# Performance work log

Measured on AMD Instinct MI355X. Metric: run time of the kernel, lower is better.

The kernel has to match this reference:

```python
import jax, jax.numpy as jnp
import numpy as np

H_DIM = 1024
HEAD_SIZE = 1024


def setup_inputs() -> dict:
    key = jax.random.key(0)
    ks = jax.random.split(key, 7)
    s = 1.0 / np.sqrt(H_DIM)
    x = jax.random.normal(ks[0], (4, 4096, H_DIM), dtype=jnp.float32)
    Wq = jax.random.uniform(ks[1], (H_DIM, HEAD_SIZE), jnp.float32, -s, s)
    bq = jax.random.uniform(ks[2], (HEAD_SIZE,), jnp.float32, -s, s)
    Wk = jax.random.uniform(ks[3], (H_DIM, HEAD_SIZE), jnp.float32, -s, s)
    bk = jax.random.uniform(ks[4], (HEAD_SIZE,), jnp.float32, -s, s)
    Wv = jax.random.uniform(ks[5], (H_DIM, HEAD_SIZE), jnp.float32, -s, s)
    bv = jax.random.uniform(ks[6], (HEAD_SIZE,), jnp.float32, -s, s)
    return {"x": x, "Wq": Wq, "bq": bq, "Wk": Wk, "bk": bk, "Wv": Wv, "bv": bv}


def reference(x, Wq, bq, Wk, bk, Wv, bv):
    B, S, _ = x.shape
    q = x @ Wq + bq  # [B,S,hs]
    k = x @ Wk + bk
    v = x @ Wv + bv
    scores = jnp.einsum('bqd,bkd->bqk', q, k)  # [B,S,S]
    causal = jnp.tril(jnp.ones((S, S), dtype=bool))
    scores = jnp.where(causal, scores, -jnp.inf)
    # original divides after masking; -inf stays -inf so math is identical
    w = jax.nn.softmax(scores / jnp.sqrt(jnp.float32(HEAD_SIZE)), axis=-1)
    # dropout p=0.0 -> identity
    return jnp.einsum('bqk,bkd->bqd', w, v)
```

## Files before the change

kernel.cpp:

```cpp
#include <hip/hip_runtime.h>
#include <stdint.h>

typedef _Float16 f16;
typedef _Float16 v8h __attribute__((ext_vector_type(8)));
typedef _Float16 v4h __attribute__((ext_vector_type(4)));
typedef float v4f __attribute__((ext_vector_type(4)));

#define LOG2E 1.44269504088896340736f
#define PT 16384

__device__ __forceinline__ void gll16(const void* g, void* l) {
  __builtin_amdgcn_global_load_lds((__attribute__((address_space(1))) void*)g,
                                   (__attribute__((address_space(3))) void*)l,
                                   16, 0, 0);
}

__device__ __forceinline__ int xcd_swz(int p, int chunk) {
  return (p & 7) * chunk + (p >> 3);
}

__global__ void k_cvt_x(const float* __restrict__ x, f16* __restrict__ xh, int n4) {
  int i = blockIdx.x * blockDim.x + threadIdx.x;
  if (i >= n4) return;
  float4 v = ((const float4*)x)[i];
  v4h o;
  o[0] = (f16)v.x; o[1] = (f16)v.y; o[2] = (f16)v.z; o[3] = (f16)v.w;
  ((v4h*)xh)[i] = o;
}

__global__ void k_cvt_wt(const float* __restrict__ Wq, const float* __restrict__ Wk,
                         const float* __restrict__ Wv, f16* __restrict__ Wt) {
  __shared__ f16 tile[64][65];
  int z = blockIdx.z;
  const float* W = (z == 0) ? Wq : (z == 1) ? Wk : Wv;
  int k0 = blockIdx.y * 64, n0 = blockIdx.x * 64;
  int t = threadIdx.x;
  int r = t >> 4, c4 = t & 15;
  for (int i = 0; i < 4; ++i) {
    int row = r + i * 16;
    float4 v = *(const float4*)&W[(size_t)(k0 + row) * 1024 + n0 + c4 * 4];
    tile[c4 * 4 + 0][row] = (f16)v.x;
    tile[c4 * 4 + 1][row] = (f16)v.y;
    tile[c4 * 4 + 2][row] = (f16)v.z;
    tile[c4 * 4 + 3][row] = (f16)v.w;
  }
  __syncthreads();
  f16* out = Wt + (size_t)z * 1048576;
  for (int i = 0; i < 4; ++i) {
    int n = r + i * 16;
    v4h o;
    o[0] = tile[n][c4 * 4 + 0];
    o[1] = tile[n][c4 * 4 + 1];
    o[2] = tile[n][c4 * 4 + 2];
    o[3] = tile[n][c4 * 4 + 3];
    *(v4h*)&out[(size_t)(n0 + n) * 1024 + k0 + c4 * 4] = o;
  }
}

__global__ __launch_bounds__(256) void k_qkv(
    const f16* __restrict__ xh,
    const f16* __restrict__ Wt,
    const float* __restrict__ bq, const float* __restrict__ bk, const float* __restrict__ bv,
    f16* __restrict__ q, f16* __restrict__ k, f16* __restrict__ vT) {
  __shared__ __align__(16) f16 As[128 * 32];
  __shared__ __align__(16) f16 Bs[128 * 32];
  int p = blockIdx.x + 8 * (blockIdx.y + 128 * blockIdx.z);
  int l = xcd_swz(p, 384);
  int mt = l / 24;
  int rem = l - mt * 24;
  int z = rem >> 3;
  int nt = rem & 7;
  int m0 = mt * 128, n0 = nt * 128;
  const f16* B = Wt + (size_t)z * 1048576;
  const float* bias = (z == 0) ? bq : (z == 1) ? bk : bv;
  int tid = threadIdx.x;
  int lane = tid & 63, wave = tid >> 6;
  int quad = lane >> 4, l15 = lane & 15;
  int wm = (wave & 1) * 64, wn = (wave >> 1) * 64;
  v4f acc[4][4] = {};

  for (int kk = 0; kk < 1024; kk += 32) {
    __syncthreads();
    for (int h = 0; h < 2; ++h) {
      int s = h * 256 + tid;
      int row = s >> 2, pos = s & 3;
      int c = pos ^ (row & 3);
      gll16(&xh[(size_t)(m0 + row) * 1024 + kk + c * 8], &As[(h * 256 + wave * 64) * 8]);
    }
    for (int h = 0; h < 2; ++h) {
      int s = h * 256 + tid;
      int row = s >> 2, pos = s & 3;
      int c = pos ^ (row & 3);
      gll16(&B[(size_t)(n0 + row) * 1024 + kk + c * 8], &Bs[(h * 256 + wave * 64) * 8]);
    }
    __syncthreads();
    v8h a[4], bf[4];
    for (int i = 0; i < 4; ++i) {
      int rowa = wm + i * 16 + l15;
      int pa = quad ^ (rowa & 3);
      a[i] = *(const v8h*)&As[rowa * 32 + pa * 8];
      int rowb = wn + i * 16 + l15;
      int pb = quad ^ (rowb & 3);
      bf[i] = *(const v8h*)&Bs[rowb * 32 + pb * 8];
    }
    for (int i = 0; i < 4; ++i)
      for (int j = 0; j < 4; ++j)
        acc[i][j] = __builtin_amdgcn_mfma_f32_16x16x32_f16(a[i], bf[j], acc[i][j], 0, 0, 0);
  }

  if (z < 2) {
    f16* out = (z == 0) ? q : k;
    float scale = (z == 0) ? 0.03125f : 1.0f;
    for (int j = 0; j < 4; ++j) {
      int n = n0 + wn + j * 16 + l15;
      float bia = bias[n];
      for (int i = 0; i < 4; ++i) {
        int mb = m0 + wm + i * 16 + quad * 4;
        for (int r = 0; r < 4; ++r)
          out[(size_t)(mb + r) * 1024 + n] = (f16)((acc[i][j][r] + bia) * scale);
      }
    }
  } else {
    for (int j = 0; j < 4; ++j) {
      int n = n0 + wn + j * 16 + l15;
      float bia = bias[n];
      for (int i = 0; i < 4; ++i) {
        int m = m0 + wm + i * 16 + quad * 4;
        int bb = m >> 12, s = m & 4095;
        v4h o;
        for (int r = 0; r < 4; ++r) o[r] = (f16)(acc[i][j][r] + bia);
        *(v4h*)&vT[((size_t)bb * 1024 + n) * 4096 + s] = o;
      }
    }
  }
}

__global__ void k_zero(float* __restrict__ p) {
  p[blockIdx.x * 256 + threadIdx.x] = 0.f;
}

__global__ __launch_bounds__(256) void k_sgemm(
    const f16* __restrict__ q, const f16* __restrict__ kmat,
    f16* __restrict__ P, float* __restrict__ rowsum, int b0) {
  __shared__ __align__(16) f16 As[128 * 32];
  __shared__ __align__(16) f16 Bs[128 * 32];
  int p = blockIdx.x + 528 * blockIdx.y;
  int l = xcd_swz(p, 132);
  int i = (l >= 528) ? l - 528 : l;
  int bb = (l >= 528) ? 1 : 0;
  int b = b0 * 2 + bb;
  int mt = (int)((sqrtf(8.f * i + 1.f) - 1.f) * 0.5f);
  while ((mt + 1) * (mt + 2) / 2 <= i) ++mt;
  while (mt * (mt + 1) / 2 > i) --mt;
  int nt = i - mt * (mt + 1) / 2;
  const f16* A = q + ((size_t)b * 4096 + (size_t)mt * 128) * 1024;
  const f16* B = kmat + ((size_t)b * 4096 + (size_t)nt * 128) * 1024;
  f16* Pt = P + (size_t)bb * 528 * PT + (size_t)i * PT;

  int tid = threadIdx.x;
  int lane = tid & 63, wave = tid >> 6;
  int quad = lane >> 4, l15 = lane & 15;
  int wm = (wave & 1) * 64, wn = (wave >> 1) * 64;
  v4f acc[4][4] = {};

  for (int kk = 0; kk < 1024; kk += 32) {
    __syncthreads();
    for (int h = 0; h < 2; ++h) {
      int s = h * 256 + tid;
      int row = s >> 2, pos = s & 3;
      int c = pos ^ (row & 3);
      gll16(&A[(size_t)row * 1024 + kk + c * 8], &As[(h * 256 + wave * 64) * 8]);
    }
    for (int h = 0; h < 2; ++h) {
      int s = h * 256 + tid;
      int row = s >> 2, pos = s & 3;
      int c = pos ^ (row & 3);
      gll16(&B[(size_t)row * 1024 + kk + c * 8], &Bs[(h * 256 + wave * 64) * 8]);
    }
    __syncthreads();
    v8h a[4], bf[4];
    for (int ii = 0; ii < 4; ++ii) {
      int rowa = wm + ii * 16 + l15;
      int pa = quad ^ (rowa & 3);
      a[ii] = *(const v8h*)&As[rowa * 32 + pa * 8];
      int rowb = wn + ii * 16 + l15;
      int pb = quad ^ (rowb & 3);
      bf[ii] = *(const v8h*)&Bs[rowb * 32 + pb * 8];
    }
    for (int ii = 0; ii < 4; ++ii)
      for (int j = 0; j < 4; ++j)
        acc[ii][j] = __builtin_amdgcn_mfma_f32_16x16x32_f16(a[ii], bf[j], acc[ii][j], 0, 0, 0);
  }

  bool diag = (nt == mt);
  float* rsb = rowsum + (size_t)b * 4096 + mt * 128;
  for (int ii = 0; ii < 4; ++ii) {
    int rl = wm + ii * 16 + quad * 4;
    for (int r = 0; r < 4; ++r) {
      int row_l = rl + r;
      float rs = 0.f;
      for (int j = 0; j < 4; ++j) {
        int col_l = wn + j * 16 + l15;
        float pv = __builtin_amdgcn_exp2f(acc[ii][j][r] * LOG2E);
        if (diag && col_l > row_l) pv = 0.f;
        Pt[(size_t)row_l * 128 + col_l] = (f16)pv;
        rs += pv;
      }
      rs += __shfl_xor(rs, 1, 64);
      rs += __shfl_xor(rs, 2, 64);
      rs += __shfl_xor(rs, 4, 64);
      rs += __shfl_xor(rs, 8, 64);
      if (l15 == 0) atomicAdd(&rsb[row_l], rs);
    }
  }
}

__global__ __launch_bounds__(256) void k_pv(
    const f16* __restrict__ P, const f16* __restrict__ vT,
    const float* __restrict__ rowsum, float* __restrict__ out, int b0) {
  __shared__ __align__(16) f16 As[128 * 64];
  __shared__ __align__(16) f16 Bs[64 * 64];
  int p = blockIdx.x + 16 * (blockIdx.y + 16 * blockIdx.z);
  int l = xcd_swz(p, 64);
  int dt = l & 15;
  int pr = (l >> 4) & 15;
  int bb = l >> 8;
  int b = b0 * 2 + bb;
  const f16* Pb = P + (size_t)bb * 528 * PT;
  const f16* Vb = vT + (size_t)b * 1024 * 4096;
  int tid = threadIdx.x;
  int lane = tid & 63, wave = tid >> 6;
  int quad = lane >> 4, l15 = lane & 15;
  int wm = (wave & 1) * 64, wn = (wave >> 1) * 32;

  for (int half = 0; half < 2; ++half) {
    int mt = half ? (31 - pr) : pr;
    size_t ptri = (size_t)mt * (mt + 1) / 2;
    v4f acc[4][2] = {};
    for (int kt = 0; kt <= mt; ++kt) {
      const f16* Ptile = Pb + (ptri + kt) * PT;
      int kabs = kt * 128;
      for (int kc = 0; kc < 128; kc += 64) {
        __syncthreads();
        for (int h = 0; h < 4; ++h) {
          int s = h * 256 + tid;
          int row = s >> 3, pos = s & 7;
          int c = pos ^ (row & 7);
          gll16(&Ptile[(size_t)row * 128 + kc + c * 8], &As[(h * 256 + wave * 64) * 8]);
        }
        for (int h = 0; h < 2; ++h) {
          int s = h * 256 + tid;
          int row = s >> 3, pos = s & 7;
          int c = pos ^ (row & 7);
          gll16(&Vb[(size_t)(dt * 64 + row) * 4096 + kabs + kc + c * 8],
                &Bs[(h * 256 + wave * 64) * 8]);
        }
        __syncthreads();
        for (int ks = 0; ks < 2; ++ks) {
          v8h a[4], bf[2];
          int lc = ks * 4 + quad;
          for (int ii = 0; ii < 4; ++ii) {
            int rowa = wm + ii * 16 + l15;
            a[ii] = *(const v8h*)&As[rowa * 64 + (lc ^ (rowa & 7)) * 8];
          }
          for (int j = 0; j < 2; ++j) {
            int rowb = wn + j * 16 + l15;
            bf[j] = *(const v8h*)&Bs[rowb * 64 + (lc ^ (rowb & 7)) * 8];
          }
          for (int ii = 0; ii < 4; ++ii)
            for (int j = 0; j < 2; ++j)
              acc[ii][j] = __builtin_amdgcn_mfma_f32_16x16x32_f16(a[ii], bf[j], acc[ii][j], 0, 0, 0);
        }
      }
    }
    const float* rsb = rowsum + (size_t)b * 4096 + mt * 128;
    float* ob = out + ((size_t)b * 4096 + (size_t)mt * 128) * 1024 + dt * 64;
    for (int ii = 0; ii < 4; ++ii) {
      int r0 = wm + ii * 16 + quad * 4;
      for (int r = 0; r < 4; ++r) {
        float inv = 1.0f / rsb[r0 + r];
        for (int j = 0; j < 2; ++j) {
          int c = wn + j * 16 + l15;
          ob[(size_t)(r0 + r) * 1024 + c] = acc[ii][j][r] * inv;
        }
      }
    }
  }
}

extern "C" void kernel_launch(void* const* d_in, const int* in_sizes, int n_in,
                              void* d_out, int out_size, void* d_ws, size_t ws_size,
                              hipStream_t stream) {
  const float* x  = (const float*)d_in[0];
  const float* Wq = (const float*)d_in[1];
  const float* bq = (const float*)d_in[2];
  const float* Wk = (const float*)d_in[3];
  const float* bk = (const float*)d_in[4];
  const float* Wv = (const float*)d_in[5];
  const float* bv = (const float*)d_in[6];
  float* out = (float*)d_out;
  char* ws = (char*)d_ws;
  f16* xh = (f16*)(ws);
  f16* Wt = (f16*)(ws + 33554432);
  f16* q  = (f16*)(ws + 39845888);
  f16* k  = (f16*)(ws + 73400320);
  f16* vT = (f16*)(ws + 106954752);
  f16* P  = (f16*)(ws);
  float* rowsum = (float*)(ws + 34603008);

  k_cvt_x<<<16384, 256, 0, stream>>>(x, xh, 4194304);
  k_cvt_wt<<<dim3(16, 16, 3), 256, 0, stream>>>(Wq, Wk, Wv, Wt);
  k_qkv<<<dim3(8, 128, 3), 256, 0, stream>>>(xh, Wt, bq, bk, bv, q, k, vT);
  k_zero<<<64, 256, 0, stream>>>(rowsum);
  for (int bp = 0; bp < 2; ++bp) {
    k_sgemm<<<dim3(528, 2), 256, 0, stream>>>(q, k, P, rowsum, bp);
    k_pv<<<dim3(16, 16, 2), 256, 0, stream>>>(P, vT, rowsum, out, bp);
  }
}
```

Measured before the change: 519.7 us.

## Rewrite QKV projection GEMM with 256x256 tiles and double-buffered async LDS loads

The QKV projection kernel now uses 512-thread blocks computing 256x256 output tiles with a K-step of 64. Global-to-LDS loads are double-buffered and overlapped with MFMA compute through vmcnt waits, and MFMA issue is bracketed by setprio. The aim is to cut per-tile synchronization stalls and raise data reuse per loaded byte. The larger tile and accumulator footprint (128 accumulators per thread, 128KB LDS) limits occupancy and adds register pressure.

```diff
diff --git a/kernel.cpp b/kernel.cpp
--- a/kernel.cpp
+++ b/kernel.cpp
@@ -57,82 +57,110 @@
   }
 }
 
-__global__ __launch_bounds__(256) void k_qkv(
+__global__ __launch_bounds__(512) void k_qkv(
     const f16* __restrict__ xh,
     const f16* __restrict__ Wt,
     const float* __restrict__ bq, const float* __restrict__ bk, const float* __restrict__ bv,
     f16* __restrict__ q, f16* __restrict__ k, f16* __restrict__ vT) {
-  __shared__ __align__(16) f16 As[128 * 32];
-  __shared__ __align__(16) f16 Bs[128 * 32];
-  int p = blockIdx.x + 8 * (blockIdx.y + 128 * blockIdx.z);
-  int l = xcd_swz(p, 384);
-  int mt = l / 24;
-  int rem = l - mt * 24;
-  int z = rem >> 3;
-  int nt = rem & 7;
-  int m0 = mt * 128, n0 = nt * 128;
-  const f16* B = Wt + (size_t)z * 1048576;
+  __shared__ __align__(16) f16 As[2][16384];
+  __shared__ __align__(16) f16 Bs[2][16384];
+  int p = blockIdx.x + 64 * (blockIdx.y + 4 * blockIdx.z);
+  int l = xcd_swz(p, 96);
+  int mt = l / 12;
+  int rem = l - mt * 12;
+  int z = rem >> 2, nt = rem & 3;
+  int m0 = mt * 256, n0 = nt * 256;
+  const f16* gA = xh + (size_t)m0 * 1024;
+  const f16* gB = Wt + (size_t)z * 1048576 + (size_t)n0 * 1024;
   const float* bias = (z == 0) ? bq : (z == 1) ? bk : bv;
   int tid = threadIdx.x;
   int lane = tid & 63, wave = tid >> 6;
   int quad = lane >> 4, l15 = lane & 15;
-  int wm = (wave & 1) * 64, wn = (wave >> 1) * 64;
-  v4f acc[4][4] = {};
-
-  for (int kk = 0; kk < 1024; kk += 32) {
-    __syncthreads();
-    for (int h = 0; h < 2; ++h) {
-      int s = h * 256 + tid;
-      int row = s >> 2, pos = s & 3;
-      int c = pos ^ (row & 3);
-      gll16(&xh[(size_t)(m0 + row) * 1024 + kk + c * 8], &As[(h * 256 + wave * 64) * 8]);
-    }
-    for (int h = 0; h < 2; ++h) {
-      int s = h * 256 + tid;
-      int row = s >> 2, pos = s & 3;
-      int c = pos ^ (row & 3);
-      gll16(&B[(size_t)(n0 + row) * 1024 + kk + c * 8], &Bs[(h * 256 + wave * 64) * 8]);
-    }
-    __syncthreads();
-    v8h a[4], bf[4];
-    for (int i = 0; i < 4; ++i) {
-      int rowa = wm + i * 16 + l15;
-      int pa = quad ^ (rowa & 3);
-      a[i] = *(const v8h*)&As[rowa * 32 + pa * 8];
-      int rowb = wn + i * 16 + l15;
-      int pb = quad ^ (rowb & 3);
-      bf[i] = *(const v8h*)&Bs[rowb * 32 + pb * 8];
-    }
-    for (int i = 0; i < 4; ++i)
-      for (int j = 0; j < 4; ++j)
-        acc[i][j] = __builtin_amdgcn_mfma_f32_16x16x32_f16(a[i], bf[j], acc[i][j], 0, 0, 0);
-  }
+  int wm = (wave >> 2) * 128, wn = (wave & 3) * 64;
+
+  int soff[4], slds[4];
+#pragma unroll
+  for (int h = 0; h < 4; ++h) {
+    int s = h * 512 + tid;
+    int row = s >> 3;
+    int c = (s & 7) ^ (row & 7);
+    soff[h] = row * 1024 + c * 8;
+    slds[h] = (h * 512 + wave * 64) * 8;
+  }
+  v4f acc[8][4] = {};
+
+#define QKV_STAGE(bb, kt_) do { int kk_ = (kt_) * 64;                      \
+    _Pragma("unroll") for (int h = 0; h < 4; ++h)                          \
+      gll16(gA + soff[h] + kk_, &As[bb][slds[h]]);                         \
+    _Pragma("unroll") for (int h = 0; h < 4; ++h)                          \
+      gll16(gB + soff[h] + kk_, &Bs[bb][slds[h]]);                         \
+  } while (0)
+
+#define QKV_COMPUTE(bb) do {                                               \
+    _Pragma("unroll") for (int ks = 0; ks < 2; ++ks) {                     \
+      int sl = ((ks * 4 + quad) ^ (l15 & 7)) * 8;                          \
+      v8h a[8], bfr[4];                                                    \
+      _Pragma("unroll") for (int i = 0; i < 8; ++i)                        \
+        a[i] = *(const v8h*)&As[bb][(wm + i * 16 + l15) * 64 + sl];        \
+      _Pragma("unroll") for (int j = 0; j < 4; ++j)                        \
+        bfr[j] = *(const v8h*)&Bs[bb][(wn + j * 16 + l15) * 64 + sl];      \
+      __builtin_amdgcn_s_setprio(1);                                       \
+      _Pragma("unroll") for (int i = 0; i < 8; ++i)                        \
+        _Pragma("unroll") for (int j = 0; j < 4; ++j)                      \
+          acc[i][j] = __builtin_amdgcn_mfma_f32_16x16x32_f16(a[i], bfr[j], acc[i][j], 0, 0, 0); \
+      __builtin_amdgcn_s_setprio(0);                                       \
+      __builtin_amdgcn_s_barrier();                                        \
+    }                                                                      \
+  } while (0)
+
+  QKV_STAGE(0, 0);
+  QKV_STAGE(1, 1);
+  int cur = 0;
+#pragma unroll 1
+  for (int kt = 0; kt < 15; ++kt) {
+    asm volatile("s_waitcnt vmcnt(8)" ::: "memory");
+    __builtin_amdgcn_s_barrier();
+    QKV_COMPUTE(cur);
+    if (kt + 2 < 16) QKV_STAGE(cur, kt + 2);
+    cur ^= 1;
+  }
+  asm volatile("s_waitcnt vmcnt(0)" ::: "memory");
+  __builtin_amdgcn_s_barrier();
+  QKV_COMPUTE(cur);
 
   if (z < 2) {
-    f16* out = (z == 0) ? q : k;
+    f16* outp = (z == 0) ? q : k;
     float scale = (z == 0) ? 0.03125f : 1.0f;
+#pragma unroll
     for (int j = 0; j < 4; ++j) {
       int n = n0 + wn + j * 16 + l15;
       float bia = bias[n];
-      for (int i = 0; i < 4; ++i) {
+#pragma unroll
+      for (int i = 0; i < 8; ++i) {
         int mb = m0 + wm + i * 16 + quad * 4;
+#pragma unroll
         for (int r = 0; r < 4; ++r)
-          out[(size_t)(mb + r) * 1024 + n] = (f16)((acc[i][j][r] + bia) * scale);
+          outp[(size_t)(mb + r) * 1024 + n] = (f16)((acc[i][j][r] + bia) * scale);
       }
     }
   } else {
+#pragma unroll
     for (int j = 0; j < 4; ++j) {
       int n = n0 + wn + j * 16 + l15;
       float bia = bias[n];
-      for (int i = 0; i < 4; ++i) {
+#pragma unroll
+      for (int i = 0; i < 8; ++i) {
         int m = m0 + wm + i * 16 + quad * 4;
         int bb = m >> 12, s = m & 4095;
         v4h o;
+#pragma unroll
         for (int r = 0; r < 4; ++r) o[r] = (f16)(acc[i][j][r] + bia);
         *(v4h*)&vT[((size_t)bb * 1024 + n) * 4096 + s] = o;
       }
     }
   }
+#undef QKV_STAGE
+#undef QKV_COMPUTE
 }
 
 __global__ void k_zero(float* __restrict__ p) {
@@ -310,7 +338,7 @@
 
   k_cvt_x<<<16384, 256, 0, stream>>>(x, xh, 4194304);
   k_cvt_wt<<<dim3(16, 16, 3), 256, 0, stream>>>(Wq, Wk, Wv, Wt);
-  k_qkv<<<dim3(8, 128, 3), 256, 0, stream>>>(xh, Wt, bq, bk, bv, q, k, vT);
+  k_qkv<<<dim3(64, 4, 3), 512, 0, stream>>>(xh, Wt, bq, bk, bv, q, k, vT);
   k_zero<<<64, 256, 0, stream>>>(rowsum);
   for (int bp = 0; bp < 2; ++bp) {
     k_sgemm<<<dim3(528, 2), 256, 0, stream>>>(q, k, P, rowsum, bp);
```

New measurement: 489.5 us. -5.8%, faster.
